# Kernel tuning notes

Hardware: AMD Instinct MI355X
Metric: run time of the kernel (lower is better)

Reference implementation:

```python
import jax, jax.numpy as jnp
import numpy as np

D = 1024
H = 16
HD = D // H
T = 2048
B = 2
WIN = 128
N_RAND = 4
LN_EPS = 1e-5


def _build_mask():
    """Replicates BigBirdBlock._create_attention_mask deterministically (seed 0).
    True = attend allowed. Local window + per-row random tokens + global first/last,
    intersected with a causal lower-triangular mask."""
    rng = np.random.default_rng(0)
    i = np.arange(T)
    half = WIN // 2
    mask = np.abs(i[:, None] - i[None, :]) <= half  # local band
    for r in range(T):
        ls, le = max(0, r - half), min(T, r + half + 1)
        # positions outside local window, excluding global tokens 0 and T-1
        avail = np.concatenate([np.arange(1, ls), np.arange(le, T - 1)])
        if avail.size:
            pick = rng.choice(avail, size=min(N_RAND, avail.size), replace=False)
            mask[r, pick] = True
    mask[0, :] = True
    mask[:, 0] = True
    mask[-1, :] = True
    mask[:, -1] = True
    mask &= (i[None, :] <= i[:, None])  # causal
    return jnp.asarray(mask)


def setup_inputs() -> dict:
    key = jax.random.key(0)
    ks = jax.random.split(key, 10)
    s = 0.02
    return {
        "x": jax.random.normal(ks[0], (B, T, D), dtype=jnp.float32),
        "mask": _build_mask(),
        "ln1_g": jnp.ones((D,), jnp.float32),
        "ln1_b": jnp.zeros((D,), jnp.float32),
        "ln2_g": jnp.ones((D,), jnp.float32),
        "ln2_b": jnp.zeros((D,), jnp.float32),
        "Wq": jax.random.normal(ks[1], (D, D), jnp.float32) * s,
        "Wk": jax.random.normal(ks[2], (D, D), jnp.float32) * s,
        "Wv": jax.random.normal(ks[3], (D, D), jnp.float32) * s,
        "Wo": jax.random.normal(ks[4], (D, D), jnp.float32) * s,
        "bo": jnp.zeros((D,), jnp.float32),
        "W1": jax.random.normal(ks[5], (D, 4 * D), jnp.float32) * s,
        "b1": jnp.zeros((4 * D,), jnp.float32),
        "W2": jax.random.normal(ks[6], (4 * D, D), jnp.float32) * s,
        "b2": jnp.zeros((D,), jnp.float32),
    }


def _ln(x, g, b):
    mu = jnp.mean(x, axis=-1, keepdims=True)
    var = jnp.mean(jnp.square(x - mu), axis=-1, keepdims=True)
    return (x - mu) * jax.lax.rsqrt(var + LN_EPS) * g + b


def reference(x, mask, ln1_g, ln1_b, ln2_g, ln2_b, Wq, Wk, Wv, Wo, bo, W1, b1, W2, b2):
    Bc, Tc, Dc = x.shape
    h = _ln(x, ln1_g, ln1_b)
    q = (h @ Wq).reshape(Bc, Tc, H, HD)
    k = (h @ Wk).reshape(Bc, Tc, H, HD)
    v = (h @ Wv).reshape(Bc, Tc, H, HD)
    scores = jnp.einsum("bqhd,bkhd->bhqk", q, k) / jnp.sqrt(jnp.asarray(HD, x.dtype))
    neg = jnp.asarray(-1e9, x.dtype)
    scores = jnp.where(mask[None, None, :, :], scores, neg)
    attn = jax.nn.softmax(scores, axis=-1)
    attn_out = jnp.einsum("bhqk,bkhd->bqhd", attn, v).reshape(Bc, Tc, Dc)
    attn_out = attn_out @ Wo + bo
    x = x + attn_out  # dropout is identity in eval mode
    h2 = _ln(x, ln2_g, ln2_b)
    ff = jax.nn.gelu(h2 @ W1 + b1, approximate=False) @ W2 + b2
    return x + ff
```

## Files before the change

kernel.cpp:

```cpp
#include <hip/hip_runtime.h>

#define T_SEQ 2048

typedef __attribute__((ext_vector_type(8))) short short8;
typedef __attribute__((ext_vector_type(4))) float f32x4;

__device__ __forceinline__ unsigned short f32_to_bf16(float f){
  unsigned int u = __float_as_uint(f);
  u += 0x7fffu + ((u>>16)&1u);
  return (unsigned short)(u>>16);
}
__device__ __forceinline__ float bf16_to_f32(unsigned short h){
  unsigned int u = ((unsigned int)h) << 16;
  return __uint_as_float(u);
}

__device__ __forceinline__ void g2l16(const void* g, void* l){
  __builtin_amdgcn_global_load_lds(
      (const __attribute__((address_space(1))) void*)g,
      (__attribute__((address_space(3))) void*)l, 16, 0, 0);
}

__device__ __forceinline__ float gelu_exact(float v){
  float s = v * 0.70710678118f;
  float a = fabsf(s);
  float t = __builtin_amdgcn_rcpf(1.f + 0.3275911f*a);
  float p = t*(0.254829592f + t*(-0.284496736f + t*(1.421413741f +
            t*(-1.453152027f + t*1.061405429f))));
  float erf_a = 1.f - p*__expf(-a*a);
  float erf_s = (s < 0.f) ? -erf_a : erf_a;
  return 0.5f*v*(1.f + erf_s);
}

__global__ __launch_bounds__(256) void packmask(const unsigned char* __restrict__ mraw,
                                                unsigned int* __restrict__ mbits){
  bool is_byte = (mraw[2049] == 1);
  int w = blockIdx.x*256 + threadIdx.x;
  int row = w >> 6, wc = w & 63;
  unsigned int bits = 0u;
  if (is_byte){
    const unsigned char* p = mraw + (size_t)row*T_SEQ + wc*32;
    #pragma unroll
    for (int j=0;j<32;j++) bits |= (p[j] ? 1u : 0u) << j;
  } else {
    const int* p = (const int*)mraw + (size_t)row*T_SEQ + wc*32;
    #pragma unroll
    for (int j=0;j<32;j++) bits |= (p[j] != 0 ? 1u : 0u) << j;
  }
  mbits[w] = bits;
}

__global__ __launch_bounds__(64) void build_cols(const unsigned int* __restrict__ mbits,
                                                 int* __restrict__ cols,
                                                 int* __restrict__ ncols){
  int qt = blockIdx.x, lane = threadIdx.x;
  unsigned int w = 0;
  for (int r=0;r<64;r++){
    int row = qt*64 + r;
    if (row == T_SEQ-1) continue;
    w |= mbits[(size_t)row*64 + lane];
  }
  int pc = __popc(w);
  int inc = pc;
  #pragma unroll
  for (int d=1; d<64; d<<=1){ int t = __shfl_up(inc, d, 64); if (lane>=d) inc += t; }
  int total = __shfl(inc, 63, 64);
  int idx = inc - pc;
  unsigned int ww = w;
  while (ww){ int b = __ffs(ww)-1; ww &= ww-1; cols[qt*2048 + idx++] = lane*32 + b; }
  for (int j = total + lane; j < 2048; j += 64) cols[qt*2048 + j] = -1;
  if (lane==0) ncols[qt] = (total + 63) & ~63;
}

__global__ __launch_bounds__(256) void build_rmask(const unsigned int* __restrict__ mbits,
                                                   const int* __restrict__ cols,
                                                   const int* __restrict__ ncols,
                                                   unsigned int* __restrict__ rmask){
  int qt = blockIdx.x, tid = threadIdx.x;
  int nw = ncols[qt] >> 5;
  for (int e = tid; e < 64*nw; e += 256){
    int row = e / nw, wj = e % nw;
    const unsigned int* mrow = mbits + (size_t)(qt*64+row)*64;
    unsigned int bits = 0;
    #pragma unroll
    for (int b=0;b<32;b++){
      int j = wj*32 + b;
      int c = cols[qt*2048 + j];
      if (c >= 0) bits |= ((mrow[c>>5] >> (c&31)) & 1u) << b;
    }
    rmask[(size_t)(qt*64+row)*64 + wj] = bits;
  }
}

__global__ __launch_bounds__(256) void transcvt(const float* __restrict__ W,
                                                unsigned short* __restrict__ WT,
                                                int K, int N){
  __shared__ float tile[32][33];
  int tx = threadIdx.x & 31, ty = threadIdx.x >> 5;
  int n0 = blockIdx.x*32, k0 = blockIdx.y*32;
  #pragma unroll
  for (int j=0;j<32;j+=8)
    tile[ty+j][tx] = W[(size_t)(k0+ty+j)*N + n0 + tx];
  __syncthreads();
  #pragma unroll
  for (int j=0;j<32;j+=8)
    WT[(size_t)(n0+ty+j)*K + k0 + tx] = f32_to_bf16(tile[tx][ty+j]);
}

__global__ __launch_bounds__(256) void ln_kernel(const float* __restrict__ x,
                                                 const float* __restrict__ g,
                                                 const float* __restrict__ b,
                                                 unsigned short* __restrict__ out){
  int row = blockIdx.x, tid = threadIdx.x;
  const float* xr = x + (size_t)row*1024;
  float4 xv = *(const float4*)(xr + tid*4);
  float s  = xv.x+xv.y+xv.z+xv.w;
  float s2 = xv.x*xv.x + xv.y*xv.y + xv.z*xv.z + xv.w*xv.w;
  #pragma unroll
  for (int d=1; d<64; d<<=1){ s += __shfl_xor(s,d,64); s2 += __shfl_xor(s2,d,64); }
  __shared__ float ls[4], ls2[4];
  int wid = tid >> 6;
  if ((tid & 63) == 0){ ls[wid]=s; ls2[wid]=s2; }
  __syncthreads();
  float tot = ls[0]+ls[1]+ls[2]+ls[3];
  float tot2= ls2[0]+ls2[1]+ls2[2]+ls2[3];
  float mu  = tot * (1.f/1024.f);
  float var = tot2 * (1.f/1024.f) - mu*mu;
  float inv = rsqrtf(var + 1e-5f);
  float4 gv = *(const float4*)(g + tid*4);
  float4 bv = *(const float4*)(b + tid*4);
  unsigned short o0 = f32_to_bf16((xv.x-mu)*inv*gv.x + bv.x);
  unsigned short o1 = f32_to_bf16((xv.y-mu)*inv*gv.y + bv.y);
  unsigned short o2 = f32_to_bf16((xv.z-mu)*inv*gv.z + bv.z);
  unsigned short o3 = f32_to_bf16((xv.w-mu)*inv*gv.w + bv.w);
  unsigned short* op = out + (size_t)row*1024 + tid*4;
  op[0]=o0; op[1]=o1; op[2]=o2; op[3]=o3;
}

template<bool GELU, bool BIAS, bool RES, bool OUTBF>
__global__ __launch_bounds__(256,4) void gemm_bt(const unsigned short* __restrict__ A,
                                                 const unsigned short* __restrict__ BT,
                                                 void* __restrict__ Cout,
                                                 const float* __restrict__ bias,
                                                 const float* __restrict__ res,
                                                 int M, int N, int K){
  __shared__ unsigned short sA[128*64];
  __shared__ unsigned short sB[128*64];
  int tid = threadIdx.x;
  int m0 = blockIdx.x*128, n0 = blockIdx.y*128;
  int wid = tid>>6, lane = tid&63;
  int wm = (wid>>1)*64, wn = (wid&1)*64;
  int l16 = lane&15, quad = lane>>4;
  int qa0 = (quad     ^ (l16&7))*8;
  int qa1 = ((quad+4) ^ (l16&7))*8;

  f32x4 acc[4][4] = {};
  for (int k0=0; k0<K; k0+=64){
    #pragma unroll
    for (int i=0;i<4;i++){
      int t = i*256 + tid;
      int row = t>>3;
      int kc = ((t&7) ^ (row&7))*8;
      int wb = i*256 + (tid & ~63);
      g2l16(A  + (size_t)(m0+row)*K + k0 + kc, sA + wb*8);
      g2l16(BT + (size_t)(n0+row)*K + k0 + kc, sB + wb*8);
    }
    __syncthreads();
    #pragma unroll
    for (int kk=0;kk<2;kk++){
      int qa = kk ? qa1 : qa0;
      short8 af[4], bf[4];
      #pragma unroll
      for (int mi=0;mi<4;mi++) af[mi] = *(const short8*)(sA + (wm+mi*16+l16)*64 + qa);
      #pragma unroll
      for (int ni=0;ni<4;ni++) bf[ni] = *(const short8*)(sB + (wn+ni*16+l16)*64 + qa);
      #pragma unroll
      for (int mi=0;mi<4;mi++)
        #pragma unroll
        for (int ni=0;ni<4;ni++)
          acc[mi][ni] = __builtin_amdgcn_mfma_f32_16x16x32_bf16(af[mi], bf[ni], acc[mi][ni], 0,0,0);
    }
    __syncthreads();
  }
  #pragma unroll
  for (int mi=0;mi<4;mi++)
    #pragma unroll
    for (int ni=0;ni<4;ni++){
      int col = n0 + wn + ni*16 + l16;
      float bval = 0.f;
      if constexpr (BIAS) bval = bias[col];
      #pragma unroll
      for (int r=0;r<4;r++){
        int row = m0 + wm + mi*16 + quad*4 + r;
        float v = acc[mi][ni][r] + bval;
        if constexpr (GELU) v = gelu_exact(v);
        if constexpr (RES)  v += res[(size_t)row*N + col];
        if constexpr (OUTBF) ((unsigned short*)Cout)[(size_t)row*N + col] = f32_to_bf16(v);
        else                 ((float*)Cout)[(size_t)row*N + col] = v;
      }
    }
}

template<bool BIAS, bool RES, bool OUTBF>
__global__ __launch_bounds__(256,2) void gemm_bt_n64(const unsigned short* __restrict__ A,
                                                     const unsigned short* __restrict__ BT,
                                                     void* __restrict__ Cout,
                                                     const float* __restrict__ bias,
                                                     const float* __restrict__ res,
                                                     int M, int N, int K){
  __shared__ unsigned short sA[128*64];
  __shared__ unsigned short sB[64*64];
  int tid = threadIdx.x;
  int m0 = blockIdx.x*128, n0 = blockIdx.y*64;
  int wid = tid>>6, lane = tid&63;
  int wm = (wid>>1)*64, wn = (wid&1)*32;
  int l16 = lane&15, quad = lane>>4;
  int qa0 = (quad     ^ (l16&7))*8;
  int qa1 = ((quad+4) ^ (l16&7))*8;

  f32x4 acc[4][2] = {};
  for (int k0=0; k0<K; k0+=64){
    #pragma unroll
    for (int i=0;i<4;i++){
      int t = i*256 + tid;
      int row = t>>3;
      int kc = ((t&7) ^ (row&7))*8;
      int wb = i*256 + (tid & ~63);
      g2l16(A + (size_t)(m0+row)*K + k0 + kc, sA + wb*8);
    }
    #pragma unroll
    for (int i=0;i<2;i++){
      int t = i*256 + tid;
      int row = t>>3;
      int kc = ((t&7) ^ (row&7))*8;
      int wb = i*256 + (tid & ~63);
      g2l16(BT + (size_t)(n0+row)*K + k0 + kc, sB + wb*8);
    }
    __syncthreads();
    #pragma unroll
    for (int kk=0;kk<2;kk++){
      int qa = kk ? qa1 : qa0;
      short8 af[4], bf[2];
      #pragma unroll
      for (int mi=0;mi<4;mi++) af[mi] = *(const short8*)(sA + (wm+mi*16+l16)*64 + qa);
      #pragma unroll
      for (int ni=0;ni<2;ni++) bf[ni] = *(const short8*)(sB + (wn+ni*16+l16)*64 + qa);
      #pragma unroll
      for (int mi=0;mi<4;mi++)
        #pragma unroll
        for (int ni=0;ni<2;ni++)
          acc[mi][ni] = __builtin_amdgcn_mfma_f32_16x16x32_bf16(af[mi], bf[ni], acc[mi][ni], 0,0,0);
    }
    __syncthreads();
  }
  #pragma unroll
  for (int mi=0;mi<4;mi++)
    #pragma unroll
    for (int ni=0;ni<2;ni++){
      int col = n0 + wn + ni*16 + l16;
      float bval = 0.f;
      if constexpr (BIAS) bval = bias[col];
      #pragma unroll
      for (int r=0;r<4;r++){
        int row = m0 + wm + mi*16 + quad*4 + r;
        float v = acc[mi][ni][r] + bval;
        if constexpr (RES)  v += res[(size_t)row*N + col];
        if constexpr (OUTBF) ((unsigned short*)Cout)[(size_t)row*N + col] = f32_to_bf16(v);
        else                 ((float*)Cout)[(size_t)row*N + col] = v;
      }
    }
}

__global__ __launch_bounds__(256,4) void attn_kernel(const unsigned short* __restrict__ qkv,
                                                     const int* __restrict__ cols,
                                                     const int* __restrict__ ncols,
                                                     const unsigned int* __restrict__ rmask,
                                                     unsigned short* __restrict__ out){
  __shared__ __align__(16) char smem[36864];
  int bh = blockIdx.y;
  int b = bh >> 4, h = bh & 15;
  int tid = threadIdx.x, wid = tid>>6, lane = tid&63;
  const int RS = 3072;
  const size_t base = (size_t)b * T_SEQ * RS;

  if (blockIdx.x == 32){
    float* sS  = (float*)smem;
    float* sOr = (float*)(smem + 8192);
    float* sRed= (float*)(smem + 16512);
    unsigned short* sQ = (unsigned short*)(smem + 16544);

    if (tid < 8)
      ((uint4*)sQ)[tid] = *(const uint4*)(qkv + base + (size_t)(T_SEQ-1)*RS + h*64 + tid*8);
    __syncthreads();
    unsigned short q16[64];
    #pragma unroll
    for (int c=0;c<8;c++) *(uint4*)(q16 + c*8) = ((const uint4*)sQ)[c];

    float lmax = -1e30f;
    #pragma unroll
    for (int i=0;i<8;i++){
      int k = tid + 256*i;
      const unsigned short* kp = qkv + base + (size_t)k*RS + 1024 + h*64;
      float acc = 0.f;
      #pragma unroll
      for (int c=0;c<8;c++){
        unsigned short kk[8];
        *(uint4*)kk = *(const uint4*)(kp + c*8);
        #pragma unroll
        for (int j=0;j<8;j++) acc += bf16_to_f32(q16[c*8+j])*bf16_to_f32(kk[j]);
      }
      float sv = acc * 0.125f;
      sS[k] = sv;
      lmax = fmaxf(lmax, sv);
    }
    #pragma unroll
    for (int d=1; d<64; d<<=1) lmax = fmaxf(lmax, __shfl_xor(lmax, d, 64));
    if (lane == 0) sRed[wid] = lmax;
    __syncthreads();
    float m = fmaxf(fmaxf(sRed[0],sRed[1]), fmaxf(sRed[2],sRed[3]));
    float lsum = 0.f;
    #pragma unroll
    for (int i=0;i<8;i++){
      int k = tid + 256*i;
      float p = __expf(sS[k] - m);
      sS[k] = p;
      lsum += p;
    }
    #pragma unroll
    for (int d=1; d<64; d<<=1) lsum += __shfl_xor(lsum, d, 64);
    if (lane == 0) sRed[4+wid] = lsum;
    __syncthreads();
    float l = sRed[4]+sRed[5]+sRed[6]+sRed[7];

    int dg = tid & 7, kl = tid >> 3;
    float o8[8] = {};
    const unsigned short* vbase = qkv + base + 2048 + h*64 + dg*8;
    #pragma unroll 4
    for (int i=0;i<64;i++){
      int k = kl + 32*i;
      float p = sS[k];
      unsigned short vv[8];
      *(uint4*)vv = *(const uint4*)(vbase + (size_t)k*RS);
      #pragma unroll
      for (int j=0;j<8;j++) o8[j] += p * bf16_to_f32(vv[j]);
    }
    #pragma unroll
    for (int j=0;j<8;j++) sOr[kl*65 + dg*8 + j] = o8[j];
    __syncthreads();
    if (tid < 64){
      float s = 0.f;
      #pragma unroll
      for (int k2=0;k2<32;k2++) s += sOr[k2*65 + tid];
      out[(size_t)(b*T_SEQ + T_SEQ-1)*1024 + h*64 + tid] = f32_to_bf16(s / l);
    }
    return;
  }

  unsigned short* sK  = (unsigned short*)smem;
  unsigned short* sVt = (unsigned short*)(smem +  9216);
  unsigned short* sX  = (unsigned short*)(smem + 18432);
  unsigned short* sP  = (unsigned short*)(smem + 27648);

  int qt = 31 - blockIdx.x;
  int l16 = lane&15, quad = lane>>4;
  int q0 = qt*64;

  const int* gcols = cols + qt*2048;
  int niter = ncols[qt] >> 6;

  int qrow = q0 + wid*16 + l16;
  const unsigned short* qptr = qkv + base + (size_t)qrow*RS + h*64;
  short8 qf0 = *(const short8*)(qptr + quad*8);
  short8 qf1 = *(const short8*)(qptr + 32 + quad*8);

  f32x4 o[4] = {};
  float m_i[4], l_i[4];
  #pragma unroll
  for (int r=0;r<4;r++){ m_i[r] = -1e30f; l_i[r] = 0.f; }

  int krow0 = tid>>3, krow1 = 32 + (tid>>3), dc = (tid&7)*8;
  int c0n = gcols[krow0], c1n = gcols[krow1];

  for (int kt=0; kt<niter; ++kt){
    int c0 = c0n < 0 ? 0 : c0n;
    int c1 = c1n < 0 ? 0 : c1n;
    const unsigned short* p0 = qkv + base + (size_t)c0*RS + 1024 + h*64 + dc;
    const unsigned short* p1 = qkv + base + (size_t)c1*RS + 1024 + h*64 + dc;
    uint4 k0 = *(const uint4*)p0;
    uint4 k1 = *(const uint4*)p1;
    uint4 v0 = *(const uint4*)(p0 + 1024);
    uint4 v1 = *(const uint4*)(p1 + 1024);
    if (kt+1 < niter){
      c0n = gcols[(kt+1)*64 + krow0];
      c1n = gcols[(kt+1)*64 + krow1];
    }
    __syncthreads();
    *(uint4*)(sK + krow0*72 + dc) = k0;
    *(uint4*)(sK + krow1*72 + dc) = k1;
    *(uint4*)(sX + krow0*72 + dc) = v0;
    *(uint4*)(sX + krow1*72 + dc) = v1;
    __syncthreads();

    #pragma unroll
    for (int pass=0; pass<2; ++pass){
      int dg = pass*4 + wid;
      unsigned short v8[8];
      *(uint4*)v8 = *(const uint4*)(sX + lane*72 + dg*8);
      #pragma unroll
      for (int j=0;j<8;j++) sVt[(dg*8+j)*72 + lane] = v8[j];
    }

    f32x4 s[4];
    #pragma unroll
    for (int nt=0;nt<4;nt++){
      f32x4 z = {};
      short8 kb0 = *(const short8*)(sK + (nt*16+l16)*72 + quad*8);
      short8 kb1 = *(const short8*)(sK + (nt*16+l16)*72 + 32 + quad*8);
      z = __builtin_amdgcn_mfma_f32_16x16x32_bf16(qf0, kb0, z, 0,0,0);
      z = __builtin_amdgcn_mfma_f32_16x16x32_bf16(qf1, kb1, z, 0,0,0);
      s[nt] = z;
    }

    float rowmax[4];
    #pragma unroll
    for (int r=0;r<4;r++){
      int rowin = wid*16 + quad*4 + r;
      const unsigned int* mrow = rmask + (size_t)(qt*64+rowin)*64 + kt*2;
      unsigned long long m64 = (unsigned long long)mrow[0] |
                               ((unsigned long long)mrow[1] << 32);
      float rm = -1e30f;
      #pragma unroll
      for (int nt=0;nt<4;nt++){
        int c6 = nt*16 + l16;
        bool ok = (m64 >> c6) & 1ull;
        float v = ok ? s[nt][r]*0.125f : -1e30f;
        s[nt][r] = v;
        rm = fmaxf(rm, v);
      }
      rowmax[r] = rm;
    }
    #pragma unroll
    for (int r=0;r<4;r++){
      float v = rowmax[r];
      #pragma unroll
      for (int d=1; d<16; d<<=1) v = fmaxf(v, __shfl_xor(v,d,64));
      rowmax[r] = v;
    }
    float alpha[4];
    #pragma unroll
    for (int r=0;r<4;r++){
      float mnew = fmaxf(m_i[r], rowmax[r]);
      alpha[r] = __expf(m_i[r] - mnew);
      m_i[r] = mnew;
    }
    #pragma unroll
    for (int nt=0;nt<4;nt++)
      #pragma unroll
      for (int r=0;r<4;r++)
        s[nt][r] = __expf(s[nt][r] - m_i[r]);
    #pragma unroll
    for (int r=0;r<4;r++){
      float v = s[0][r]+s[1][r]+s[2][r]+s[3][r];
      #pragma unroll
      for (int d=1; d<16; d<<=1) v += __shfl_xor(v,d,64);
      l_i[r] = l_i[r]*alpha[r] + v;
    }
    unsigned short* sPw = sP + wid*16*72;
    #pragma unroll
    for (int nt=0;nt<4;nt++)
      #pragma unroll
      for (int r=0;r<4;r++)
        sPw[(quad*4+r)*72 + nt*16 + l16] = f32_to_bf16(s[nt][r]);
    short8 p0f = *(const short8*)(sPw + l16*72 + quad*8);
    short8 p1f = *(const short8*)(sPw + l16*72 + 32 + quad*8);
    #pragma unroll
    for (int nt=0;nt<4;nt++)
      #pragma unroll
      for (int r=0;r<4;r++)
        o[nt][r] *= alpha[r];
    __syncthreads();
    #pragma unroll
    for (int nt=0;nt<4;nt++){
      short8 vb0 = *(const short8*)(sVt + (nt*16+l16)*72 + quad*8);
      short8 vb1 = *(const short8*)(sVt + (nt*16+l16)*72 + 32 + quad*8);
      o[nt] = __builtin_amdgcn_mfma_f32_16x16x32_bf16(p0f, vb0, o[nt], 0,0,0);
      o[nt] = __builtin_amdgcn_mfma_f32_16x16x32_bf16(p1f, vb1, o[nt], 0,0,0);
    }
  }
  #pragma unroll
  for (int nt=0;nt<4;nt++)
    #pragma unroll
    for (int r=0;r<4;r++){
      int row = q0 + wid*16 + quad*4 + r;
      if (row == T_SEQ-1) continue;
      int col = h*64 + nt*16 + l16;
      out[(size_t)(b*T_SEQ + row)*1024 + col] = f32_to_bf16(o[nt][r] / l_i[r]);
    }
}

extern "C" void kernel_launch(void* const* d_in, const int* in_sizes, int n_in,
                              void* d_out, int out_size, void* d_ws, size_t ws_size,
                              hipStream_t stream) {
  const float* x     = (const float*)d_in[0];
  const unsigned char* mask = (const unsigned char*)d_in[1];
  const float* ln1_g = (const float*)d_in[2];
  const float* ln1_b = (const float*)d_in[3];
  const float* ln2_g = (const float*)d_in[4];
  const float* ln2_b = (const float*)d_in[5];
  const float* Wq = (const float*)d_in[6];
  const float* Wk = (const float*)d_in[7];
  const float* Wv = (const float*)d_in[8];
  const float* Wo = (const float*)d_in[9];
  const float* bo = (const float*)d_in[10];
  const float* W1 = (const float*)d_in[11];
  const float* b1 = (const float*)d_in[12];
  const float* W2 = (const float*)d_in[13];
  const float* b2 = (const float*)d_in[14];
  float* out = (float*)d_out;

  char* ws = (char*)d_ws;
  unsigned short* wqkvT = (unsigned short*)(ws);
  unsigned short* woT   = (unsigned short*)(ws + 6291456);
  unsigned short* w1T   = (unsigned short*)(ws + 8388608);
  unsigned short* w2T   = (unsigned short*)(ws + 16777216);
  unsigned short* h_bf  = (unsigned short*)(ws + 25165824);
  unsigned short* qkv   = (unsigned short*)(ws + 33554432);
  unsigned short* aout  = (unsigned short*)(ws + 58720256);
  unsigned int*   mbits = (unsigned int*)(ws + 67108864);
  int*            cols  = (int*)(ws + 67633152);
  int*            ncols = (int*)(ws + 67895296);
  unsigned int*   rmask = (unsigned int*)(ws + 67895424);
  unsigned short* ff1   = qkv;

  packmask<<<512,256,0,stream>>>(mask, mbits);
  build_cols<<<32,64,0,stream>>>(mbits, cols, ncols);
  build_rmask<<<32,256,0,stream>>>(mbits, cols, ncols, rmask);
  transcvt<<<dim3(32,32),256,0,stream>>>(Wq, wqkvT,               1024, 1024);
  transcvt<<<dim3(32,32),256,0,stream>>>(Wk, wqkvT + 1024*1024,   1024, 1024);
  transcvt<<<dim3(32,32),256,0,stream>>>(Wv, wqkvT + 2*1024*1024, 1024, 1024);
  transcvt<<<dim3(32,32),256,0,stream>>>(Wo, woT,                 1024, 1024);
  transcvt<<<dim3(128,32),256,0,stream>>>(W1, w1T, 1024, 4096);
  transcvt<<<dim3(32,128),256,0,stream>>>(W2, w2T, 4096, 1024);

  ln_kernel<<<4096,256,0,stream>>>(x, ln1_g, ln1_b, h_bf);
  gemm_bt<false,false,false,true><<<dim3(32,24),256,0,stream>>>(h_bf, wqkvT, qkv, nullptr, nullptr, 4096, 3072, 1024);
  attn_kernel<<<dim3(33,32),256,0,stream>>>(qkv, cols, ncols, rmask, aout);
  gemm_bt_n64<true,true,false><<<dim3(32,16),256,0,stream>>>(aout, woT, out, bo, x, 4096, 1024, 1024);
  ln_kernel<<<4096,256,0,stream>>>(out, ln2_g, ln2_b, h_bf);
  gemm_bt<true,true,false,true><<<dim3(32,32),256,0,stream>>>(h_bf, w1T, ff1, b1, nullptr, 4096, 4096, 1024);
  gemm_bt_n64<true,true,false><<<dim3(32,16),256,0,stream>>>(ff1, w2T, out, b2, out, 4096, 1024, 4096);
}
```

Measured before the change: 371.0 us.

## Double-buffer GEMM LDS tiles with 32-wide K stages to overlap loads

```diff
diff --git a/kernel.cpp b/kernel.cpp
--- a/kernel.cpp
+++ b/kernel.cpp
@@ -144,43 +144,48 @@
                                                  const float* __restrict__ bias,
                                                  const float* __restrict__ res,
                                                  int M, int N, int K){
-  __shared__ unsigned short sA[128*64];
-  __shared__ unsigned short sB[128*64];
+  __shared__ unsigned short sA[2][128*32];
+  __shared__ unsigned short sB[2][128*32];
   int tid = threadIdx.x;
   int m0 = blockIdx.x*128, n0 = blockIdx.y*128;
   int wid = tid>>6, lane = tid&63;
   int wm = (wid>>1)*64, wn = (wid&1)*64;
   int l16 = lane&15, quad = lane>>4;
-  int qa0 = (quad     ^ (l16&7))*8;
-  int qa1 = ((quad+4) ^ (l16&7))*8;
+  int qa = (quad ^ ((l16>>1)&3))*8;
+
+  int t1 = 256 + tid;
+  int row0 = tid>>2, kc0 = ((tid&3) ^ ((row0>>1)&3))*8, wb0 = (tid & ~63);
+  int row1 = t1 >>2, kc1 = ((t1 &3) ^ ((row1>>1)&3))*8, wb1 = 256 + (tid & ~63);
+
+  auto stage = [&](int buf, int k0){
+    g2l16(A  + (size_t)(m0+row0)*K + k0 + kc0, sA[buf] + wb0*8);
+    g2l16(BT + (size_t)(n0+row0)*K + k0 + kc0, sB[buf] + wb0*8);
+    g2l16(A  + (size_t)(m0+row1)*K + k0 + kc1, sA[buf] + wb1*8);
+    g2l16(BT + (size_t)(n0+row1)*K + k0 + kc1, sB[buf] + wb1*8);
+  };
 
   f32x4 acc[4][4] = {};
+  auto compute = [&](int buf){
+    short8 af[4], bf[4];
+    #pragma unroll
+    for (int mi=0;mi<4;mi++) af[mi] = *(const short8*)(sA[buf] + (wm+mi*16+l16)*32 + qa);
+    #pragma unroll
+    for (int ni=0;ni<4;ni++) bf[ni] = *(const short8*)(sB[buf] + (wn+ni*16+l16)*32 + qa);
+    #pragma unroll
+    for (int mi=0;mi<4;mi++)
+      #pragma unroll
+      for (int ni=0;ni<4;ni++)
+        acc[mi][ni] = __builtin_amdgcn_mfma_f32_16x16x32_bf16(af[mi], bf[ni], acc[mi][ni], 0,0,0);
+  };
+
+  stage(0, 0);
   for (int k0=0; k0<K; k0+=64){
-    #pragma unroll
-    for (int i=0;i<4;i++){
-      int t = i*256 + tid;
-      int row = t>>3;
-      int kc = ((t&7) ^ (row&7))*8;
-      int wb = i*256 + (tid & ~63);
-      g2l16(A  + (size_t)(m0+row)*K + k0 + kc, sA + wb*8);
-      g2l16(BT + (size_t)(n0+row)*K + k0 + kc, sB + wb*8);
-    }
-    __syncthreads();
-    #pragma unroll
-    for (int kk=0;kk<2;kk++){
-      int qa = kk ? qa1 : qa0;
-      short8 af[4], bf[4];
-      #pragma unroll
-      for (int mi=0;mi<4;mi++) af[mi] = *(const short8*)(sA + (wm+mi*16+l16)*64 + qa);
-      #pragma unroll
-      for (int ni=0;ni<4;ni++) bf[ni] = *(const short8*)(sB + (wn+ni*16+l16)*64 + qa);
-      #pragma unroll
-      for (int mi=0;mi<4;mi++)
-        #pragma unroll
-        for (int ni=0;ni<4;ni++)
-          acc[mi][ni] = __builtin_amdgcn_mfma_f32_16x16x32_bf16(af[mi], bf[ni], acc[mi][ni], 0,0,0);
-    }
-    __syncthreads();
+    __syncthreads();
+    if (k0+32 < K) stage(1, k0+32);
+    compute(0);
+    __syncthreads();
+    if (k0+64 < K) stage(0, k0+64);
+    compute(1);
   }
   #pragma unroll
   for (int mi=0;mi<4;mi++)
@@ -208,50 +213,47 @@
                                                      const float* __restrict__ bias,
                                                      const float* __restrict__ res,
                                                      int M, int N, int K){
-  __shared__ unsigned short sA[128*64];
-  __shared__ unsigned short sB[64*64];
+  __shared__ unsigned short sA[2][128*32];
+  __shared__ unsigned short sB[2][64*32];
   int tid = threadIdx.x;
   int m0 = blockIdx.x*128, n0 = blockIdx.y*64;
   int wid = tid>>6, lane = tid&63;
   int wm = (wid>>1)*64, wn = (wid&1)*32;
   int l16 = lane&15, quad = lane>>4;
-  int qa0 = (quad     ^ (l16&7))*8;
-  int qa1 = ((quad+4) ^ (l16&7))*8;
+  int qa = (quad ^ ((l16>>1)&3))*8;
+
+  int t1 = 256 + tid;
+  int row0 = tid>>2, kc0 = ((tid&3) ^ ((row0>>1)&3))*8, wb0 = (tid & ~63);
+  int row1 = t1 >>2, kc1 = ((t1 &3) ^ ((row1>>1)&3))*8, wb1 = 256 + (tid & ~63);
+
+  auto stage = [&](int buf, int k0){
+    g2l16(A  + (size_t)(m0+row0)*K + k0 + kc0, sA[buf] + wb0*8);
+    g2l16(A  + (size_t)(m0+row1)*K + k0 + kc1, sA[buf] + wb1*8);
+    g2l16(BT + (size_t)(n0+row0)*K + k0 + kc0, sB[buf] + wb0*8);
+  };
 
   f32x4 acc[4][2] = {};
+  auto compute = [&](int buf){
+    short8 af[4], bf[2];
+    #pragma unroll
+    for (int mi=0;mi<4;mi++) af[mi] = *(const short8*)(sA[buf] + (wm+mi*16+l16)*32 + qa);
+    #pragma unroll
+    for (int ni=0;ni<2;ni++) bf[ni] = *(const short8*)(sB[buf] + (wn+ni*16+l16)*32 + qa);
+    #pragma unroll
+    for (int mi=0;mi<4;mi++)
+      #pragma unroll
+      for (int ni=0;ni<2;ni++)
+        acc[mi][ni] = __builtin_amdgcn_mfma_f32_16x16x32_bf16(af[mi], bf[ni], acc[mi][ni], 0,0,0);
+  };
+
+  stage(0, 0);
   for (int k0=0; k0<K; k0+=64){
-    #pragma unroll
-    for (int i=0;i<4;i++){
-      int t = i*256 + tid;
-      int row = t>>3;
-      int kc = ((t&7) ^ (row&7))*8;
-      int wb = i*256 + (tid & ~63);
-      g2l16(A + (size_t)(m0+row)*K + k0 + kc, sA + wb*8);
-    }
-    #pragma unroll
-    for (int i=0;i<2;i++){
-      int t = i*256 + tid;
-      int row = t>>3;
-      int kc = ((t&7) ^ (row&7))*8;
-      int wb = i*256 + (tid & ~63);
-      g2l16(BT + (size_t)(n0+row)*K + k0 + kc, sB + wb*8);
-    }
-    __syncthreads();
-    #pragma unroll
-    for (int kk=0;kk<2;kk++){
-      int qa = kk ? qa1 : qa0;
-      short8 af[4], bf[2];
-      #pragma unroll
-      for (int mi=0;mi<4;mi++) af[mi] = *(const short8*)(sA + (wm+mi*16+l16)*64 + qa);
-      #pragma unroll
-      for (int ni=0;ni<2;ni++) bf[ni] = *(const short8*)(sB + (wn+ni*16+l16)*64 + qa);
-      #pragma unroll
-      for (int mi=0;mi<4;mi++)
-        #pragma unroll
-        for (int ni=0;ni<2;ni++)
-          acc[mi][ni] = __builtin_amdgcn_mfma_f32_16x16x32_bf16(af[mi], bf[ni], acc[mi][ni], 0,0,0);
-    }
-    __syncthreads();
+    __syncthreads();
+    if (k0+32 < K) stage(1, k0+32);
+    compute(0);
+    __syncthreads();
+    if (k0+64 < K) stage(0, k0+64);
+    compute(1);
   }
   #pragma unroll
   for (int mi=0;mi<4;mi++)
```

Result: slower. 387.2 us (+4.4%).
